# Kernel optimization log

Hardware: AMD Instinct MI355X
Metric: run time of the kernel (lower is better)

The kernel has to match this reference:

```python
import jax, jax.numpy as jnp
import numpy as np

B, S, D, H, E, TOPK = 8, 1024, 512, 2048, 8, 2


def setup_inputs() -> dict:
    key = jax.random.key(0)
    ks = jax.random.split(key, 7)
    scale = 0.02
    return {
        "x": jax.random.normal(ks[0], (B, S, D), jnp.float32),
        "gate_w": jax.random.normal(ks[1], (D, E), jnp.float32) * scale,
        "gate_b": jnp.zeros((E,), jnp.float32),
        "w1": jax.random.normal(ks[2], (E, D, H), jnp.float32) * scale,
        "b1": jnp.zeros((E, H), jnp.float32),
        "w2": jax.random.normal(ks[3], (E, H, D), jnp.float32) * scale,
        "b2": jnp.zeros((E, D), jnp.float32),
    }


def reference(x, gate_w, gate_b, w1, b1, w2, b2):
    # ---- MoE transformer MLP (fastmoe FMoETransformerMLP, NaiveGate) ----
    xt = x.reshape(-1, D)                       # [T, D], T = B*S tokens
    logits = xt @ gate_w + gate_b               # [T, E]
    top_val, top_idx = jax.lax.top_k(logits, TOPK)  # [T, k]
    score = jax.nn.softmax(top_val, axis=-1)    # softmax over the k selected logits

    y = jnp.zeros_like(xt)
    # Loop over the small fixed expert set; each token's combine weight for
    # expert e is the sum of its top-k scores routed to e (0 if not selected).
    for e in range(E):
        w_tok = jnp.sum(score * (top_idx == e), axis=-1)        # [T]
        h = jax.nn.gelu(xt @ w1[e] + b1[e], approximate=False)  # [T, H]
        y = y + w_tok[:, None] * (h @ w2[e] + b2[e])            # [T, D]

    y = y.reshape(B, S, D)
    # Outer model: log_softmax over seq of channel-summed features
    return jax.nn.log_softmax(jnp.sum(y, axis=2), axis=1)       # [B, S]
```

## Files before the change

### kernel.cpp

```cpp
#include <hip/hip_runtime.h>
#include <hip/hip_bf16.h>
#include <math.h>

#define T_TOK 8192
#define DIM   512
#define NEXP  8
#define HID   2048
#define NBAT  8
#define SEQ   1024

typedef short  short8 __attribute__((ext_vector_type(8)));
typedef float  f32x4  __attribute__((ext_vector_type(4)));

__device__ __forceinline__ unsigned short f2bf(float f) {
    union { float f; unsigned int u; } v; v.f = f;
    unsigned int u = v.u;
    unsigned int r = u + 0x7FFFu + ((u >> 16) & 1u);
    return (unsigned short)(r >> 16);
}

__device__ __forceinline__ float gelu_f(float v) {
    float v2 = v * v;
    float w = v * (-2.302344f - 0.102955f * v2);
    return v / (1.f + __builtin_amdgcn_exp2f(w));
}

__global__ void prep_gate_k(const float* __restrict__ w1, unsigned short* __restrict__ w1t,
                            const float* __restrict__ w2, const float* __restrict__ b2,
                            float* __restrict__ w2sum, float* __restrict__ b2sum,
                            int* __restrict__ counts,
                            const float* __restrict__ x, const float* __restrict__ gw,
                            const float* __restrict__ gb,
                            unsigned short* __restrict__ xb,
                            int* __restrict__ eidx, float* __restrict__ esc0,
                            float* __restrict__ esc1) {
    int bid = blockIdx.x;
    int tid = threadIdx.x;
    int wave = tid >> 6, lane = tid & 63;
    if (bid < 2048) {
        __shared__ unsigned short tile[64][65];
        int e = bid >> 8, r = bid & 255;
        int d0 = (r & 7) * 64, h0 = (r >> 3) * 64;
        const float* src = w1 + (size_t)e * DIM * HID;
        #pragma unroll
        for (int pass = 0; pass < 4; ++pass) {
            int dr = pass * 16 + (tid >> 4);
            int hc = (tid & 15) * 4;
            float4 v = *(const float4*)(src + (size_t)(d0 + dr) * HID + h0 + hc);
            tile[hc + 0][dr] = f2bf(v.x);
            tile[hc + 1][dr] = f2bf(v.y);
            tile[hc + 2][dr] = f2bf(v.z);
            tile[hc + 3][dr] = f2bf(v.w);
        }
        __syncthreads();
        unsigned short* dst = w1t + (size_t)e * HID * DIM;
        #pragma unroll
        for (int pass = 0; pass < 4; ++pass) {
            int hr = pass * 16 + (tid >> 4);
            int dc = (tid & 15) * 4;
            ushort4 o;
            o.x = tile[hr][dc];     o.y = tile[hr][dc + 1];
            o.z = tile[hr][dc + 2]; o.w = tile[hr][dc + 3];
            *(ushort4*)(dst + (size_t)(h0 + hr) * DIM + d0 + dc) = o;
        }
    } else if (bid < 4096) {
        int t = (bid - 2048) * 4 + wave;
        const float* xp = x + (size_t)t * DIM;
        unsigned short* xbp = xb + (size_t)t * DIM;
        float acc[8] = {0, 0, 0, 0, 0, 0, 0, 0};
        #pragma unroll
        for (int it = 0; it < 8; ++it) {
            int d = it * 64 + lane;
            float xv = xp[d];
            xbp[d] = f2bf(xv);
            float4 g0 = *(const float4*)(gw + d * 8);
            float4 g1 = *(const float4*)(gw + d * 8 + 4);
            acc[0] += xv * g0.x; acc[1] += xv * g0.y; acc[2] += xv * g0.z; acc[3] += xv * g0.w;
            acc[4] += xv * g1.x; acc[5] += xv * g1.y; acc[6] += xv * g1.z; acc[7] += xv * g1.w;
        }
        #pragma unroll
        for (int e = 0; e < 8; ++e) {
            float s = acc[e];
            #pragma unroll
            for (int off = 32; off >= 1; off >>= 1) s += __shfl_xor(s, off);
            acc[e] = s + gb[e];
        }
        float v0 = -1e30f, v1 = -1e30f; int i0 = 0, i1 = 0;
        #pragma unroll
        for (int e = 0; e < 8; ++e) {
            float v = acc[e];
            if (v > v0) { v1 = v0; i1 = i0; v0 = v; i0 = e; }
            else if (v > v1) { v1 = v; i1 = e; }
        }
        float e1 = expf(v1 - v0);
        float inv = 1.f / (1.f + e1);
        if (lane == 0) {
            eidx[t] = i0 | (i1 << 4);
            esc0[t] = inv;
            esc1[t] = e1 * inv;
        }
    } else if (bid < 8192) {
        int row = (bid - 4096) * 4 + wave;
        const float* p = w2 + (size_t)row * DIM;
        float4 a = *(const float4*)(p + lane * 4);
        float4 b = *(const float4*)(p + 256 + lane * 4);
        float s = a.x + a.y + a.z + a.w + b.x + b.y + b.z + b.w;
        #pragma unroll
        for (int off = 32; off >= 1; off >>= 1) s += __shfl_xor(s, off);
        if (lane == 0) w2sum[row] = s;
    } else {
        if (tid < 8) counts[tid] = 0;
        for (int r = wave; r < NEXP; r += 4) {
            const float* p = b2 + (size_t)r * DIM;
            float s = 0.f;
            for (int i = lane; i < DIM; i += 64) s += p[i];
            #pragma unroll
            for (int off = 32; off >= 1; off >>= 1) s += __shfl_xor(s, off);
            if (lane == 0) b2sum[r] = s;
        }
    }
}

__global__ __launch_bounds__(1024) void route_k(
    const int* __restrict__ eidx, const float* __restrict__ esc0,
    const float* __restrict__ esc1, const float* __restrict__ b2sum,
    int* __restrict__ counts,
    int* __restrict__ ptok, float* __restrict__ pscore,
    float* __restrict__ s_partial) {
    int tid = threadIdx.x;
    int t = blockIdx.x * 1024 + tid;
    int wv = tid >> 6, lane = tid & 63;
    int pk = eidx[t];
    int i0 = pk & 0xf, i1 = (pk >> 4) & 0xf;
    float s0 = esc0[t], s1 = esc1[t];

    s_partial[t] = s0 * b2sum[i0] + s1 * b2sum[i1];

    __shared__ int waveCnt[16][8];
    __shared__ int waveBase[16][8];

    unsigned long long m0[8], m1[8];
    #pragma unroll
    for (int e = 0; e < 8; ++e) {
        m0[e] = __ballot(i0 == e);
        m1[e] = __ballot(i1 == e);
    }
    if (lane < 8) {
        int c = 0;
        #pragma unroll
        for (int e = 0; e < 8; ++e)
            if (lane == e) c = __popcll(m0[e]) + __popcll(m1[e]);
        waveCnt[wv][lane] = c;
    }
    __syncthreads();
    if (tid < 8) {
        int e = tid;
        int total = 0;
        #pragma unroll
        for (int w = 0; w < 16; ++w) total += waveCnt[w][e];
        int base = atomicAdd(&counts[e], total);
        int run = base;
        #pragma unroll
        for (int w = 0; w < 16; ++w) {
            waveBase[w][e] = run;
            run += waveCnt[w][e];
        }
    }
    __syncthreads();

    unsigned long long lt = (1ULL << lane) - 1ULL;
    int slot0 = 0, slot1 = 0;
    #pragma unroll
    for (int e = 0; e < 8; ++e) {
        if (i0 == e) slot0 = waveBase[wv][e] + __popcll(m0[e] & lt);
        if (i1 == e) slot1 = waveBase[wv][e] + __popcll(m0[e]) + __popcll(m1[e] & lt);
    }
    ptok[i0 * T_TOK + slot0] = t;  pscore[i0 * T_TOK + slot0] = s0;
    ptok[i1 * T_TOK + slot1] = t;  pscore[i1 * T_TOK + slot1] = s1;
}

#define GPTR(p) (const __attribute__((address_space(1))) void*)(p)
#define LPTR(p) (__attribute__((address_space(3))) void*)(p)

__global__ __launch_bounds__(256, 4) void moe_gemm_k(
    const unsigned short* __restrict__ xb, const unsigned short* __restrict__ w1t,
    const float* __restrict__ b1, const float* __restrict__ w2sum,
    const int* __restrict__ counts, const int* __restrict__ ptok,
    const float* __restrict__ pscore, float* __restrict__ s_partial) {

    int flat = blockIdx.x + (int)blockIdx.y * 135;
    int xcd = flat & 7;
    int s = flat >> 3;
    int bx = s >> 1;
    int hBase = (xcd * 2 + (s & 1)) * 128;

    int e = 8, rowBase = 0, accT = 0;
    #pragma unroll
    for (int i = 0; i < 8; ++i) {
        int nt = (counts[i] + 127) >> 7;
        if (e == 8 && bx < accT + nt) { e = i; rowBase = (bx - accT) * 128; }
        accT += nt;
    }
    if (e == 8) return;
    int n_e = counts[e];

    __shared__ unsigned short A_s[2][128 * 32];
    __shared__ unsigned short B_s[2][128 * 32];
    __shared__ int   tokLds[128];
    __shared__ float scoreLds[128];

    int tid = threadIdx.x;
    int wave = tid >> 6, lane = tid & 63;

    if (tid < 128) {
        int r = rowBase + tid;
        bool valid = r < n_e;
        tokLds[tid]   = valid ? ptok[e * T_TOK + r]   : 0;
        scoreLds[tid] = valid ? pscore[e * T_TOK + r] : 0.f;
    }
    __syncthreads();

    const unsigned short* gA[2];
    const unsigned short* gB[2];
    int lo[2];
    #pragma unroll
    for (int i = 0; i < 2; ++i) {
        int c = (i * 4 + wave) * 64 + lane;
        int stripe = c >> 3, slot = c & 7;
        int sp = slot ^ (stripe & 7);
        int row = 2 * stripe + (sp >> 2);
        int j = (sp & 3) * 8;
        gA[i] = xb + (size_t)tokLds[row] * DIM + j;
        gB[i] = w1t + ((size_t)e * HID + hBase + row) * DIM + j;
        lo[i] = c * 8;
    }

    int wm = wave >> 1, wn = wave & 1;
    int quad = lane >> 4, col = lane & 15;

    f32x4 acc[4][4];
    #pragma unroll
    for (int m = 0; m < 4; ++m)
        #pragma unroll
        for (int n = 0; n < 4; ++n)
            acc[m][n] = (f32x4){0.f, 0.f, 0.f, 0.f};

    int rslot = (((col & 1) << 2) | quad) ^ ((col >> 1) & 7);
    int aOff = (wm * 32 + (col >> 1)) * 64 + rslot * 8;
    int bOff = (wn * 32 + (col >> 1)) * 64 + rslot * 8;

    #pragma unroll
    for (int i = 0; i < 2; ++i) {
        __builtin_amdgcn_global_load_lds(GPTR(gA[i]), LPTR(&A_s[0][lo[i]]), 16, 0, 0);
        __builtin_amdgcn_global_load_lds(GPTR(gB[i]), LPTR(&B_s[0][lo[i]]), 16, 0, 0);
    }
    #pragma unroll
    for (int i = 0; i < 2; ++i) {
        __builtin_amdgcn_global_load_lds(GPTR(gA[i] + 32), LPTR(&A_s[1][lo[i]]), 16, 0, 0);
        __builtin_amdgcn_global_load_lds(GPTR(gB[i] + 32), LPTR(&B_s[1][lo[i]]), 16, 0, 0);
    }

    #pragma unroll
    for (int kk = 0; kk < 16; ++kk) {
        const int cur = kk & 1;
        if (kk < 15) { asm volatile("s_waitcnt vmcnt(4)" ::: "memory"); }
        else         { asm volatile("s_waitcnt vmcnt(0)" ::: "memory"); }
        __builtin_amdgcn_s_barrier();

        short8 af[4], bf[4];
        const unsigned short* aB = &A_s[cur][aOff];
        const unsigned short* bB = &B_s[cur][bOff];
        #pragma unroll
        for (int m = 0; m < 4; ++m) af[m] = *(const short8*)(aB + m * 512);
        #pragma unroll
        for (int n = 0; n < 4; ++n) bf[n] = *(const short8*)(bB + n * 512);
        asm volatile("s_waitcnt lgkmcnt(0)" ::: "memory");
        __builtin_amdgcn_s_barrier();

        if (kk < 14) {
            int ko = (kk + 2) * 32;
            #pragma unroll
            for (int i = 0; i < 2; ++i) {
                __builtin_amdgcn_global_load_lds(GPTR(gA[i] + ko), LPTR(&A_s[cur][lo[i]]), 16, 0, 0);
                __builtin_amdgcn_global_load_lds(GPTR(gB[i] + ko), LPTR(&B_s[cur][lo[i]]), 16, 0, 0);
            }
        }
        __builtin_amdgcn_sched_barrier(0);

        __builtin_amdgcn_s_setprio(1);
        #pragma unroll
        for (int m = 0; m < 4; ++m)
            #pragma unroll
            for (int n = 0; n < 4; ++n)
                acc[m][n] = __builtin_amdgcn_mfma_f32_16x16x32_bf16(af[m], bf[n], acc[m][n], 0, 0, 0);
        __builtin_amdgcn_s_setprio(0);
    }

    const float* b1e = b1 + e * HID;
    const float* w2e = w2sum + e * HID;
    float bias[4], wsum[4];
    #pragma unroll
    for (int n = 0; n < 4; ++n) {
        int h = hBase + wn * 64 + n * 16 + col;
        bias[n] = b1e[h];
        wsum[n] = w2e[h];
    }
    #pragma unroll
    for (int m = 0; m < 4; ++m) {
        float rp0 = 0.f, rp1 = 0.f, rp2 = 0.f, rp3 = 0.f;
        #pragma unroll
        for (int n = 0; n < 4; ++n) {
            rp0 += gelu_f(acc[m][n][0] + bias[n]) * wsum[n];
            rp1 += gelu_f(acc[m][n][1] + bias[n]) * wsum[n];
            rp2 += gelu_f(acc[m][n][2] + bias[n]) * wsum[n];
            rp3 += gelu_f(acc[m][n][3] + bias[n]) * wsum[n];
        }
        #pragma unroll
        for (int off = 8; off >= 1; off >>= 1) {
            rp0 += __shfl_xor(rp0, off);
            rp1 += __shfl_xor(rp1, off);
            rp2 += __shfl_xor(rp2, off);
            rp3 += __shfl_xor(rp3, off);
        }
        if (col < 4) {
            float mine = (col == 0) ? rp0 : (col == 1) ? rp1 : (col == 2) ? rp2 : rp3;
            int rl = wm * 64 + m * 16 + quad * 4 + col;
            int r = rowBase + rl;
            if (r < n_e)
                atomicAdd(&s_partial[tokLds[rl]], scoreLds[rl] * mine);
        }
    }
}

__global__ void lsm_k(const float* __restrict__ s, float* __restrict__ out) {
    int b = blockIdx.x, tid = threadIdx.x;
    int wave = tid >> 6, lane = tid & 63;
    __shared__ float red[4];
    const float* sp = s + (size_t)b * SEQ;
    float v[4];
    #pragma unroll
    for (int i = 0; i < 4; ++i) v[i] = sp[tid + i * 256];
    float m = fmaxf(fmaxf(v[0], v[1]), fmaxf(v[2], v[3]));
    #pragma unroll
    for (int off = 32; off >= 1; off >>= 1) m = fmaxf(m, __shfl_xor(m, off));
    if (lane == 0) red[wave] = m;
    __syncthreads();
    m = fmaxf(fmaxf(red[0], red[1]), fmaxf(red[2], red[3]));
    __syncthreads();
    float t = 0.f;
    #pragma unroll
    for (int i = 0; i < 4; ++i) t += expf(v[i] - m);
    #pragma unroll
    for (int off = 32; off >= 1; off >>= 1) t += __shfl_xor(t, off);
    if (lane == 0) red[wave] = t;
    __syncthreads();
    t = red[0] + red[1] + red[2] + red[3];
    float L = m + logf(t);
    #pragma unroll
    for (int i = 0; i < 4; ++i) out[(size_t)b * SEQ + tid + i * 256] = v[i] - L;
}

extern "C" void kernel_launch(void* const* d_in, const int* in_sizes, int n_in,
                              void* d_out, int out_size, void* d_ws, size_t ws_size,
                              hipStream_t stream) {
    const float* x  = (const float*)d_in[0];
    const float* gw = (const float*)d_in[1];
    const float* gb = (const float*)d_in[2];
    const float* w1 = (const float*)d_in[3];
    const float* b1 = (const float*)d_in[4];
    const float* w2 = (const float*)d_in[5];
    const float* b2 = (const float*)d_in[6];
    float* out = (float*)d_out;

    char* ws = (char*)d_ws;
    int*   counts    = (int*)  (ws + 0);
    float* b2sum     = (float*)(ws + 1280);
    float* s_partial = (float*)(ws + 1536);
    float* w2sum     = (float*)(ws + 34304);
    int*   ptok      = (int*)  (ws + 99840);
    float* pscore    = (float*)(ws + 361984);
    int*   eidx      = (int*)  (ws + 624128);
    float* esc0      = (float*)(ws + 656896);
    float* esc1      = (float*)(ws + 689664);
    unsigned short* xb  = (unsigned short*)(ws + 722432);
    unsigned short* w1t = (unsigned short*)(ws + 9111040);

    prep_gate_k<<<8193, 256, 0, stream>>>(w1, w1t, w2, b2, w2sum, b2sum, counts,
                                          x, gw, gb, xb, eidx, esc0, esc1);
    route_k<<<NEXP, 1024, 0, stream>>>(eidx, esc0, esc1, b2sum, counts, ptok, pscore, s_partial);
    moe_gemm_k<<<dim3(135, 16), 256, 0, stream>>>(xb, w1t, b1, w2sum, counts, ptok, pscore, s_partial);
    lsm_k<<<NBAT, 256, 0, stream>>>(s_partial, out);
}
```

Measured before the change: 182.5 us.

## Pre-swizzle W1 into MFMA fragment order and load B directly to registers

```diff
diff --git a/kernel.cpp b/kernel.cpp
--- a/kernel.cpp
+++ b/kernel.cpp
@@ -25,7 +25,7 @@
     return v / (1.f + __builtin_amdgcn_exp2f(w));
 }
 
-__global__ void prep_gate_k(const float* __restrict__ w1, unsigned short* __restrict__ w1t,
+__global__ void prep_gate_k(const float* __restrict__ w1, unsigned short* __restrict__ w1f,
                             const float* __restrict__ w2, const float* __restrict__ b2,
                             float* __restrict__ w2sum, float* __restrict__ b2sum,
                             int* __restrict__ counts,
@@ -38,7 +38,7 @@
     int tid = threadIdx.x;
     int wave = tid >> 6, lane = tid & 63;
     if (bid < 2048) {
-        __shared__ unsigned short tile[64][65];
+        __shared__ unsigned short tile[64][68];
         int e = bid >> 8, r = bid & 255;
         int d0 = (r & 7) * 64, h0 = (r >> 3) * 64;
         const float* src = w1 + (size_t)e * DIM * HID;
@@ -53,15 +53,19 @@
             tile[hc + 3][dr] = f2bf(v.w);
         }
         __syncthreads();
-        unsigned short* dst = w1t + (size_t)e * HID * DIM;
-        #pragma unroll
-        for (int pass = 0; pass < 4; ++pass) {
-            int hr = pass * 16 + (tid >> 4);
-            int dc = (tid & 15) * 4;
-            ushort4 o;
-            o.x = tile[hr][dc];     o.y = tile[hr][dc + 1];
-            o.z = tile[hr][dc + 2]; o.w = tile[hr][dc + 3];
-            *(ushort4*)(dst + (size_t)(h0 + hr) * DIM + d0 + dc) = o;
+        int l = tid & 63, q = l >> 4, c = l & 15;
+        int kk0 = (r & 7) * 2, g0 = (r >> 3) * 4;
+        #pragma unroll
+        for (int pi = 0; pi < 2; ++pi) {
+            int sub = pi * 4 + wave;
+            int kk2 = sub >> 2, g2 = sub & 3;
+            const unsigned short* tp = &tile[g2 * 16 + c][kk2 * 32 + q * 8];
+            ushort4 a = *(const ushort4*)(tp);
+            ushort4 b = *(const ushort4*)(tp + 4);
+            unsigned short* dst = w1f +
+                ((size_t)(e * 128 + g0 + g2) * 16 + kk0 + kk2) * 512 + l * 8;
+            *(ushort4*)(dst)     = a;
+            *(ushort4*)(dst + 4) = b;
         }
     } else if (bid < 4096) {
         int t = (bid - 2048) * 4 + wave;
@@ -183,7 +187,7 @@
 #define LPTR(p) (__attribute__((address_space(3))) void*)(p)
 
 __global__ __launch_bounds__(256, 4) void moe_gemm_k(
-    const unsigned short* __restrict__ xb, const unsigned short* __restrict__ w1t,
+    const unsigned short* __restrict__ xb, const unsigned short* __restrict__ w1f,
     const float* __restrict__ b1, const float* __restrict__ w2sum,
     const int* __restrict__ counts, const int* __restrict__ ptok,
     const float* __restrict__ pscore, float* __restrict__ s_partial) {
@@ -205,7 +209,6 @@
     int n_e = counts[e];
 
     __shared__ unsigned short A_s[2][128 * 32];
-    __shared__ unsigned short B_s[2][128 * 32];
     __shared__ int   tokLds[128];
     __shared__ float scoreLds[128];
 
@@ -221,7 +224,6 @@
     __syncthreads();
 
     const unsigned short* gA[2];
-    const unsigned short* gB[2];
     int lo[2];
     #pragma unroll
     for (int i = 0; i < 2; ++i) {
@@ -231,7 +233,6 @@
         int row = 2 * stripe + (sp >> 2);
         int j = (sp & 3) * 8;
         gA[i] = xb + (size_t)tokLds[row] * DIM + j;
-        gB[i] = w1t + ((size_t)e * HID + hBase + row) * DIM + j;
         lo[i] = c * 8;
     }
 
@@ -247,43 +248,39 @@
 
     int rslot = (((col & 1) << 2) | quad) ^ ((col >> 1) & 7);
     int aOff = (wm * 32 + (col >> 1)) * 64 + rslot * 8;
-    int bOff = (wn * 32 + (col >> 1)) * 64 + rslot * 8;
-
-    #pragma unroll
-    for (int i = 0; i < 2; ++i) {
+
+    const unsigned short* bp = w1f +
+        (size_t)(e * 128 + (hBase >> 4) + wn * 4) * 8192 + lane * 8;
+    short8 bf[4];
+
+    #pragma unroll
+    for (int n = 0; n < 4; ++n) bf[n] = *(const short8*)(bp + n * 8192);
+    #pragma unroll
+    for (int i = 0; i < 2; ++i)
         __builtin_amdgcn_global_load_lds(GPTR(gA[i]), LPTR(&A_s[0][lo[i]]), 16, 0, 0);
-        __builtin_amdgcn_global_load_lds(GPTR(gB[i]), LPTR(&B_s[0][lo[i]]), 16, 0, 0);
-    }
-    #pragma unroll
-    for (int i = 0; i < 2; ++i) {
+    #pragma unroll
+    for (int i = 0; i < 2; ++i)
         __builtin_amdgcn_global_load_lds(GPTR(gA[i] + 32), LPTR(&A_s[1][lo[i]]), 16, 0, 0);
-        __builtin_amdgcn_global_load_lds(GPTR(gB[i] + 32), LPTR(&B_s[1][lo[i]]), 16, 0, 0);
-    }
 
     #pragma unroll
     for (int kk = 0; kk < 16; ++kk) {
         const int cur = kk & 1;
-        if (kk < 15) { asm volatile("s_waitcnt vmcnt(4)" ::: "memory"); }
-        else         { asm volatile("s_waitcnt vmcnt(0)" ::: "memory"); }
+        if (kk == 0) { asm volatile("s_waitcnt vmcnt(2)" ::: "memory"); }
+        else         { asm volatile("s_waitcnt vmcnt(6)" ::: "memory"); }
         __builtin_amdgcn_s_barrier();
 
-        short8 af[4], bf[4];
+        short8 af[4];
         const unsigned short* aB = &A_s[cur][aOff];
-        const unsigned short* bB = &B_s[cur][bOff];
         #pragma unroll
         for (int m = 0; m < 4; ++m) af[m] = *(const short8*)(aB + m * 512);
-        #pragma unroll
-        for (int n = 0; n < 4; ++n) bf[n] = *(const short8*)(bB + n * 512);
         asm volatile("s_waitcnt lgkmcnt(0)" ::: "memory");
         __builtin_amdgcn_s_barrier();
 
         if (kk < 14) {
             int ko = (kk + 2) * 32;
             #pragma unroll
-            for (int i = 0; i < 2; ++i) {
+            for (int i = 0; i < 2; ++i)
                 __builtin_amdgcn_global_load_lds(GPTR(gA[i] + ko), LPTR(&A_s[cur][lo[i]]), 16, 0, 0);
-                __builtin_amdgcn_global_load_lds(GPTR(gB[i] + ko), LPTR(&B_s[cur][lo[i]]), 16, 0, 0);
-            }
         }
         __builtin_amdgcn_sched_barrier(0);
 
@@ -294,6 +291,12 @@
             for (int n = 0; n < 4; ++n)
                 acc[m][n] = __builtin_amdgcn_mfma_f32_16x16x32_bf16(af[m], bf[n], acc[m][n], 0, 0, 0);
         __builtin_amdgcn_s_setprio(0);
+
+        if (kk < 15) {
+            #pragma unroll
+            for (int n = 0; n < 4; ++n)
+                bf[n] = *(const short8*)(bp + n * 8192 + (kk + 1) * 512);
+        }
     }
 
     const float* b1e = b1 + e * HID;
@@ -383,11 +386,11 @@
     float* esc0      = (float*)(ws + 656896);
     float* esc1      = (float*)(ws + 689664);
     unsigned short* xb  = (unsigned short*)(ws + 722432);
-    unsigned short* w1t = (unsigned short*)(ws + 9111040);
-
-    prep_gate_k<<<8193, 256, 0, stream>>>(w1, w1t, w2, b2, w2sum, b2sum, counts,
+    unsigned short* w1f = (unsigned short*)(ws + 9111040);
+
+    prep_gate_k<<<8193, 256, 0, stream>>>(w1, w1f, w2, b2, w2sum, b2sum, counts,
                                           x, gw, gb, xb, eidx, esc0, esc1);
     route_k<<<NEXP, 1024, 0, stream>>>(eidx, esc0, esc1, b2sum, counts, ptok, pscore, s_partial);
-    moe_gemm_k<<<dim3(135, 16), 256, 0, stream>>>(xb, w1t, b1, w2sum, counts, ptok, pscore, s_partial);
+    moe_gemm_k<<<dim3(135, 16), 256, 0, stream>>>(xb, w1f, b1, w2sum, counts, ptok, pscore, s_partial);
     lsm_k<<<NBAT, 256, 0, stream>>>(s_partial, out);
 }
```

Measured after the change: 184.2 us. Within noise of the previous version (+0.9%).
